# Optimization experiments

Measured on AMD Instinct MI355X. Metric: run time of the kernel, lower is better.

The kernel has to match this reference:

```python
import math
import jax, jax.numpy as jnp
import numpy as np

C = 1.0          # Poincare ball curvature
NUM_HEADS = 8
EPS = 1e-15

def _beta(a, b):
    # Beta function via lgamma (python float constant)
    return math.exp(math.lgamma(a) + math.lgamma(b) - math.lgamma(a + b))

def h_linear(x, z, r, c=C):
    """HNN++ Poincare fully-connected layer (hypll HLinear).
    x: [..., in] points in the ball; z: [in, out] tangent weights; r: [out] bias."""
    sc = math.sqrt(c)
    x2 = jnp.sum(x * x, axis=-1, keepdims=True)
    lam = 2.0 / (1.0 - c * x2)                                # conformal factor
    zn = jnp.maximum(jnp.linalg.norm(z, axis=0), EPS)          # [out]
    inner = x @ z                                              # [..., out]
    two_scr = 2.0 * sc * r
    d = (2.0 * zn / sc) * jnp.arcsinh(
        (sc * inner * lam / zn) * jnp.cosh(two_scr) - (lam - 1.0) * jnp.sinh(two_scr)
    )
    w = jnp.sinh(sc * d) / sc
    return w / (1.0 + jnp.sqrt(1.0 + c * jnp.sum(w * w, axis=-1, keepdims=True)))

def pairwise_dist(q, k, c=C):
    """Poincare distance d(q,k) = arccosh(1 + 2c|q-k|^2 / ((1-c|q|^2)(1-c|k|^2))) / sqrt(c).
    q,k: [B,H,S,hd] -> [B,H,S,S]."""
    q2 = jnp.sum(q * q, axis=-1)
    k2 = jnp.sum(k * k, axis=-1)
    qk = jnp.einsum('bhqd,bhkd->bhqk', q, k)
    diff2 = jnp.maximum(q2[..., :, None] + k2[..., None, :] - 2.0 * qk, 0.0)
    denom = (1.0 - c * q2)[..., :, None] * (1.0 - c * k2)[..., None, :]
    arg = 1.0 + 2.0 * c * diff2 / denom
    return jnp.arccosh(jnp.maximum(arg, 1.0 + 1e-7)) / math.sqrt(c)

def midpoint(v, w, c=C):
    """Weighted Mobius gyromidpoint: m = 1/2 (x) (sum w*lam*x / sum w*(lam-1)).
    v: [B,H,Sk,hd], w: [B,H,Sq,Sk] -> [B,H,Sq,hd]."""
    v2 = jnp.sum(v * v, axis=-1)                      # [B,H,Sk]
    lam = 2.0 / (1.0 - c * v2)
    num = jnp.einsum('bhqk,bhkd->bhqd', w * lam[..., None, :], v)
    den = jnp.maximum(jnp.einsum('bhqk,bhk->bhq', w, lam - 1.0), EPS)[..., None]
    g = num / den                                     # gyromidpoint pre-scaling
    sc = math.sqrt(c)
    gn = jnp.maximum(jnp.linalg.norm(g, axis=-1, keepdims=True), EPS)
    t = jnp.tanh(0.5 * jnp.arctanh(jnp.clip(sc * gn, 0.0, 1.0 - 1e-7)))
    return (t / sc) * g / gn

def _forward(query, key, value, Wq, bq, Wk, bk, Wv, bv, scale_tau, scale_gamma):
    B, S, E = query.shape
    H = NUM_HEADS
    hd = E // H
    # hyperbolic q/k/v projections, then split into heads: [B,H,S,hd]
    q = h_linear(query, Wq, bq).reshape(B, S, H, hd).transpose(0, 2, 1, 3)
    k = h_linear(key, Wk, bk).reshape(B, S, H, hd).transpose(0, 2, 1, 3)
    v = h_linear(value, Wv, bv).reshape(B, S, H, hd).transpose(0, 2, 1, 3)
    # similarity = -dist/tau - gamma with tau = exp(-scale_tau)
    sim = -pairwise_dist(q, k) * jnp.exp(scale_tau[0]) - scale_gamma[0]
    causal = jnp.triu(jnp.ones((S, S), dtype=bool), k=1)
    sim = jnp.where(causal, -jnp.inf, sim)
    w = jnp.exp(sim)                                  # 'exp' attention activation
    agg = midpoint(v, w)                              # [B,H,S,hd]
    agg = agg.transpose(0, 2, 1, 3).reshape(B, S, E)
    # HNN++ beta-concatenation of the per-head ball points
    scale = _beta(E / 2.0, 0.5) / _beta(hd / 2.0, 0.5)
    return agg * scale

def setup_inputs() -> dict:
    root = jax.random.key(0)
    ks = jax.random.split(root, 8)
    B, S, E = 1, 2048, 512
    s = 0.02  # keep points well inside the unit ball
    return {
        'query': s * jax.random.normal(ks[0], (B, S, E), jnp.float32),
        'key':   s * jax.random.normal(ks[1], (B, S, E), jnp.float32),
        'value': s * jax.random.normal(ks[2], (B, S, E), jnp.float32),
        'Wq': s * jax.random.normal(ks[3], (E, E), jnp.float32),
        'Wk': s * jax.random.normal(ks[4], (E, E), jnp.float32),
        'Wv': s * jax.random.normal(ks[5], (E, E), jnp.float32),
        'bq': jnp.zeros((E,), jnp.float32),
        'bk': jnp.zeros((E,), jnp.float32),
        'bv': jnp.zeros((E,), jnp.float32),
        'scale_tau': jnp.zeros((1,), jnp.float32),
        'scale_gamma': jnp.zeros((1,), jnp.float32),
    }

def reference(query, key, value, Wq, Wk, Wv, bq, bk, bv, scale_tau, scale_gamma):
    return _forward(query, key, value, Wq, bq, Wk, bk, Wv, bv, scale_tau, scale_gamma)
```

## Files before the change

kernel.cpp:

```cpp
#include <hip/hip_runtime.h>
#include <cmath>

#define H 8
#define SEQ 2048
#define EDIM 512
#define HD 64
#define EPSF 1e-15f

typedef short bf16x8 __attribute__((ext_vector_type(8)));
typedef float f32x4 __attribute__((ext_vector_type(4)));

#define ZN_OFF    16
#define STATS_OFF (ZN_OFF + 24 * EDIM)
#define CQ_OFF    (STATS_OFF + 3 * H * SEQ)
#define IK_OFF    (CQ_OFF + H * SEQ)
#define PX2_OFF   (IK_OFF + H * SEQ)
#define U16_OFF   (PX2_OFF + 12288 + 16)
#define WT_U16    0
#define QKVB_U16  (WT_U16 + 3 * EDIM * EDIM)
#define VT_U16    (QKVB_U16 + 3 * SEQ * EDIM)
#define U16_TOTAL (VT_U16 + H * 80 * SEQ)
#define BIG_OFF   (U16_OFF + U16_TOTAL / 2 + 16)
#define PART_U16S (8 * 32 * 8 * 4 * 1280)
#define ACC_FLOATS  (H * SEQ * 80)

__device__ __forceinline__ float bf2f(unsigned short u){
  union { unsigned int i; float f; } v; v.i = ((unsigned int)u) << 16; return v.f;
}
__device__ __forceinline__ unsigned short f2bf(float f){
  union { float f; unsigned int i; } v; v.f = f;
  unsigned int x = v.i;
  unsigned int r = (x + 0x7fffu + ((x >> 16) & 1u)) >> 16;
  return (unsigned short)r;
}

__device__ __forceinline__ int detect_f32(const unsigned short* __restrict__ q){
  const int l = threadIdx.x & 63;
  float mx = 0.f;
  #pragma unroll
  for (int j = 0; j < 4; ++j) mx = fmaxf(mx, fabsf(bf2f(q[l * 4 + j])));
  #pragma unroll
  for (int m = 32; m >= 1; m >>= 1) mx = fmaxf(mx, __shfl_xor(mx, m, 64));
  return mx > 1000.f;
}

__global__ __launch_bounds__(256) void wcvt_kernel(
    const void* __restrict__ Wq, const void* __restrict__ Wk, const void* __restrict__ Wv,
    const unsigned short* __restrict__ qprobe,
    unsigned short* __restrict__ WT, float* __restrict__ zn)
{
  const int p = blockIdx.y;
  const int bi = blockIdx.x >> 3, bo = blockIdx.x & 7;
  const void* W = (p == 0) ? Wq : ((p == 1) ? Wk : Wv);
  const int t = threadIdx.x;
  const int isf32 = detect_f32(qprobe);
  __shared__ float tile[64][65];

  #pragma unroll
  for (int j = 0; j < 16; ++j){
    int idx = t + 256 * j;
    int il = idx >> 6, ol = idx & 63;
    float val;
    if (isf32) val = ((const float*)W)[(size_t)(bi * 64 + il) * EDIM + bo * 64 + ol];
    else       val = bf2f(((const unsigned short*)W)[(size_t)(bi * 64 + il) * EDIM + bo * 64 + ol]);
    tile[il][ol] = val;
  }
  __syncthreads();
  if (t < 64){
    float s = 0.f;
    #pragma unroll 8
    for (int i = 0; i < 64; ++i){ float v = tile[i][t]; s += v * v; }
    zn[((size_t)(bi * 3 + p)) * EDIM + bo * 64 + t] = s;
  }
  #pragma unroll
  for (int j = 0; j < 16; ++j){
    int idx = t + 256 * j;
    int ol = idx >> 6, il = idx & 63;
    WT[((size_t)p * EDIM + bo * 64 + ol) * EDIM + bi * 64 + il] = f2bf(tile[il][ol]);
  }
}

__global__ __launch_bounds__(256) void hlin_gemm_kernel(
    const void* __restrict__ Xq, const void* __restrict__ Xk, const void* __restrict__ Xv,
    const unsigned short* __restrict__ WT, const unsigned short* __restrict__ qprobe,
    unsigned short* __restrict__ partC, float* __restrict__ partX2)
{
  const int p = blockIdx.y;
  const int rg = blockIdx.x >> 1;
  const int kslice = blockIdx.x & 1;
  const void* X = (p == 0) ? Xq : ((p == 1) ? Xk : Xv);
  const int r0 = rg * 16;
  const int t  = threadIdx.x;
  const int w = t >> 6, lane = t & 63;
  const int col = lane & 15, quad = lane >> 4;
  const int isf32 = detect_f32(qprobe);
  const int koff = kslice * 256;

  const unsigned short* WTb = WT + ((size_t)p * EDIM + w * 128 + col) * EDIM + koff;
  const float* Xf = (const float*)X + (size_t)(r0 + col) * EDIM + koff;
  const unsigned short* Xh = (const unsigned short*)X + (size_t)(r0 + col) * EDIM + koff;

  f32x4 acc[8];
  #pragma unroll
  for (int nt = 0; nt < 8; ++nt) acc[nt] = (f32x4){0.f, 0.f, 0.f, 0.f};
  float x2part = 0.f;

  bf16x8 caf, naf;
  bf16x8 cbf[8], nbf[8];
  {
    if (isf32){
      float4 xa = *(const float4*)&Xf[quad * 8];
      float4 xb = *(const float4*)&Xf[quad * 8 + 4];
      float xv[8] = {xa.x, xa.y, xa.z, xa.w, xb.x, xb.y, xb.z, xb.w};
      #pragma unroll
      for (int j = 0; j < 8; ++j){ caf[j] = (short)f2bf(xv[j]); x2part += xv[j] * xv[j]; }
    } else {
      caf = *(const bf16x8*)&Xh[quad * 8];
      #pragma unroll
      for (int j = 0; j < 8; ++j){ float xv = bf2f((unsigned short)caf[j]); x2part += xv * xv; }
    }
    #pragma unroll
    for (int nt = 0; nt < 8; ++nt)
      cbf[nt] = *(const bf16x8*)&WTb[(size_t)nt * 16 * EDIM + quad * 8];
  }

  for (int ks = 0; ks < 8; ++ks){
    if (ks + 1 < 8){
      const int off = (ks + 1) * 32 + quad * 8;
      if (isf32){
        float4 xa = *(const float4*)&Xf[off];
        float4 xb = *(const float4*)&Xf[off + 4];
        float xv[8] = {xa.x, xa.y, xa.z, xa.w, xb.x, xb.y, xb.z, xb.w};
        #pragma unroll
        for (int j = 0; j < 8; ++j){ naf[j] = (short)f2bf(xv[j]); x2part += xv[j] * xv[j]; }
      } else {
        naf = *(const bf16x8*)&Xh[off];
        #pragma unroll
        for (int j = 0; j < 8; ++j){ float xv = bf2f((unsigned short)naf[j]); x2part += xv * xv; }
      }
      #pragma unroll
      for (int nt = 0; nt < 8; ++nt)
        nbf[nt] = *(const bf16x8*)&WTb[(size_t)nt * 16 * EDIM + off];
    }
    #pragma unroll
    for (int nt = 0; nt < 8; ++nt)
      acc[nt] = __builtin_amdgcn_mfma_f32_16x16x32_bf16(caf, cbf[nt], acc[nt], 0, 0, 0);
    if (ks + 1 < 8){
      caf = naf;
      #pragma unroll
      for (int nt = 0; nt < 8; ++nt) cbf[nt] = nbf[nt];
    }
  }
  x2part += __shfl_xor(x2part, 16, 64);
  x2part += __shfl_xor(x2part, 32, 64);

  const size_t base = ((size_t)(p * 128 + rg) * 2 + kslice) * 8192;
  #pragma unroll
  for (int nt = 0; nt < 8; ++nt)
    #pragma unroll
    for (int r = 0; r < 4; ++r)
      partC[base + (size_t)(quad * 4 + r) * 512 + w * 128 + nt * 16 + col] = f2bf(acc[nt][r]);
  if (w == 0 && quad == 0)
    partX2[((size_t)(p * 128 + rg) * 2 + kslice) * 16 + col] = x2part;
}

__global__ __launch_bounds__(256) void hlin_fin_kernel(
    const unsigned short* __restrict__ partC, const float* __restrict__ partX2,
    const void* __restrict__ Bq, const void* __restrict__ Bk, const void* __restrict__ Bv,
    const float* __restrict__ znacc, const unsigned short* __restrict__ qprobe,
    unsigned short* __restrict__ qkvb, float* __restrict__ stats,
    float* __restrict__ cqs, float* __restrict__ iks,
    unsigned short* __restrict__ VT)
{
  const int p = blockIdx.y;
  const void* Bb = (p == 0) ? Bq : ((p == 1) ? Bk : Bv);
  const int rg = blockIdx.x;
  const int r0 = rg * 16;
  const int t  = threadIdx.x;
  const int w = t >> 6, lane = t & 63;
  const int col = lane & 15, quad = lane >> 4;
  const int isf32 = detect_f32(qprobe);

  __shared__ float smem[16 * EDIM];
  __shared__ float sw2[16];

  const size_t base0 = ((size_t)(p * 128 + rg) * 2 + 0) * 8192;
  const size_t base1 = base0 + 8192;

  f32x4 acc[8];
  #pragma unroll
  for (int nt = 0; nt < 8; ++nt)
    #pragma unroll
    for (int r = 0; r < 4; ++r){
      const size_t idx = (size_t)(quad * 4 + r) * 512 + w * 128 + nt * 16 + col;
      acc[nt][r] = bf2f(partC[base0 + idx]) + bf2f(partC[base1 + idx]);
    }

  float lamr[4], lm1[4];
  #pragma unroll
  for (int r = 0; r < 4; ++r){
    const int row = quad * 4 + r;
    float x2r = partX2[((size_t)(p * 128 + rg) * 2 + 0) * 16 + row] +
                partX2[((size_t)(p * 128 + rg) * 2 + 1) * 16 + row];
    lamr[r] = 2.f / (1.f - x2r);
    lm1[r] = lamr[r] - 1.f;
  }
  #pragma unroll
  for (int nt = 0; nt < 8; ++nt){
    const int n = w * 128 + nt * 16 + col;
    float zsum = 0.f;
    #pragma unroll
    for (int bi = 0; bi < 8; ++bi)
      zsum += znacc[((size_t)(bi * 3 + p)) * EDIM + n];
    float znv = fmaxf(sqrtf(zsum), EPSF);
    float rb;
    if (isf32) rb = ((const float*)Bb)[n];
    else       rb = bf2f(((const unsigned short*)Bb)[n]);
    float e2r = __expf(2.f * rb);
    float ie2r = 1.f / e2r;
    float ch = 0.5f * (e2r + ie2r), sh = 0.5f * (e2r - ie2r);
    float izn = 1.f / znv;
    float tz = 2.f * znv;
    #pragma unroll
    for (int r = 0; r < 4; ++r){
      float a = (acc[nt][r] * lamr[r] * izn) * ch - lm1[r] * sh;
      float b = a + sqrtf(a * a + 1.f);
      float tt = __expf(tz * __logf(b));
      smem[(quad * 4 + r) * EDIM + n] = 0.5f * (tt - 1.f / tt);
    }
  }
  __syncthreads();

  {
    int row = t >> 4, l = t & 15;
    float s = 0.f;
    for (int o = l; o < EDIM; o += 16){ float wv = smem[row * EDIM + o]; s += wv * wv; }
    #pragma unroll
    for (int m = 8; m >= 1; m >>= 1) s += __shfl_xor(s, m, 16);
    if (l == 0) sw2[row] = s;
  }
  __syncthreads();

  const int o0 = 2 * t;
  const int h0 = t >> 5;
  const int d0 = o0 & 63;
  const int l5 = t & 31;
  #pragma unroll
  for (int rr = 0; rr < 16; ++rr){
    float inv = 1.f / (1.f + sqrtf(1.f + sw2[rr]));
    unsigned short b0 = f2bf(smem[rr * EDIM + o0] * inv);
    unsigned short b1 = f2bf(smem[rr * EDIM + o0 + 1] * inv);
    float r0v = bf2f(b0), r1v = bf2f(b1);
    int s = r0 + rr;
    unsigned int* dst = (unsigned int*)&qkvb[(((size_t)p * H + h0) * SEQ + s) * HD + d0];
    *dst = (unsigned int)b0 | ((unsigned int)b1 << 16);
    float ss = r0v * r0v + r1v * r1v;
    #pragma unroll
    for (int m = 16; m >= 1; m >>= 1) ss += __shfl_xor(ss, m, 64);
    if (p == 2){
      float lam = 2.f / (1.f - ss);
      VT[((size_t)h0 * 80 + d0) * SEQ + s]     = f2bf(r0v * lam);
      VT[((size_t)h0 * 80 + d0 + 1) * SEQ + s] = f2bf(r1v * lam);
      if (l5 < 16)
        VT[((size_t)h0 * 80 + 64 + l5) * SEQ + s] = (l5 == 0) ? f2bf(lam - 1.f) : 0;
    }
    if (l5 == 0){
      stats[((size_t)p * H + h0) * SEQ + s] = ss;
      if (p == 0) cqs[(size_t)h0 * SEQ + s] = 2.f / (1.f - ss);
      if (p == 1) iks[(size_t)h0 * SEQ + s] = 1.f / (1.f - ss);
    }
  }
}

__global__ __launch_bounds__(64) void attn_kernel(
    const unsigned short* __restrict__ Qb, const unsigned short* __restrict__ Kb,
    const unsigned short* __restrict__ VT,
    const float* __restrict__ q2s_all, const float* __restrict__ k2s_all,
    const float* __restrict__ cqs_all, const float* __restrict__ iks_all,
    const void* __restrict__ tau, const void* __restrict__ gam,
    const unsigned short* __restrict__ qprobe,
    float* __restrict__ big, int use_part)
{
  const int h  = blockIdx.y;
  const int tile = 31 - (blockIdx.x >> 4);
  const int sl = (blockIdx.x >> 1) & 7;
  const int wp = blockIdx.x & 1;
  if (sl > tile) return;
  const int lane = threadIdx.x;
  const int col = lane & 15, quad = lane >> 4;
  const int q0A = tile * 64 + wp * 16;
  const int q0B = q0A + 32;

  const unsigned short* Qh  = Qb + (size_t)h * SEQ * HD;
  const unsigned short* Kh  = Kb + (size_t)h * SEQ * HD;
  const unsigned short* VTh = VT + (size_t)h * 80 * SEQ;
  const float* q2s = q2s_all + (size_t)h * SEQ;
  const float* k2s = k2s_all + (size_t)h * SEQ;
  const float* cqs = cqs_all + (size_t)h * SEQ;
  const float* iks = iks_all + (size_t)h * SEQ;

  const int isf32 = detect_f32(qprobe);
  float tauv, gamv;
  if (isf32){ tauv = ((const float*)tau)[0]; gamv = ((const float*)gam)[0]; }
  else      { tauv = bf2f(((const unsigned short*)tau)[0]);
              gamv = bf2f(((const unsigned short*)gam)[0]); }
  const float e_tau = __expf(tauv);

  const int srcA = ((quad & 1) * 2) * 16 + col;
  const int srcB = srcA + 16;
  const int tsel = quad >> 1;

  bf16x8 qfA0 = *(const bf16x8*)&Qh[(size_t)(q0A + col) * HD + quad * 8];
  bf16x8 qfA1 = *(const bf16x8*)&Qh[(size_t)(q0A + col) * HD + 32 + quad * 8];
  bf16x8 qfB0 = *(const bf16x8*)&Qh[(size_t)(q0B + col) * HD + quad * 8];
  bf16x8 qfB1 = *(const bf16x8*)&Qh[(size_t)(q0B + col) * HD + 32 + quad * 8];
  const float q2A = q2s[q0A + col], q2B = q2s[q0B + col];
  const float cqA = cqs[q0A + col], cqB = cqs[q0B + col];
  const int qmaxA = q0A + col, qmaxB = q0B + col;

  f32x4 pvA[5], pvB[5];
  #pragma unroll
  for (int nt = 0; nt < 5; ++nt){
    pvA[nt] = (f32x4){0.f, 0.f, 0.f, 0.f};
    pvB[nt] = (f32x4){0.f, 0.f, 0.f, 0.f};
  }

  const int nch = ((tile - sl) >> 3) + 1;
  const int nhalf = nch * 2;
  int kb32 = sl * 64;

  bf16x8 ckf0[2], ckf1[2], nkf0[2], nkf1[2];
  float4 ck2[2], cik[2], nk2[2], nik[2];
  #pragma unroll
  for (int tt = 0; tt < 2; ++tt){
    const int kbase = kb32 + 16 * tt;
    ckf0[tt] = *(const bf16x8*)&Kh[(size_t)(kbase + col) * HD + quad * 8];
    ckf1[tt] = *(const bf16x8*)&Kh[(size_t)(kbase + col) * HD + 32 + quad * 8];
    ck2[tt]  = *(const float4*)&k2s[kbase + quad * 4];
    cik[tt]  = *(const float4*)&iks[kbase + quad * 4];
  }

  for (int i = 0; i < nhalf; ++i){
    const int nkb32 = (i & 1) ? (kb32 + 512 - 32) : (kb32 + 32);
    const bool have_next = (i + 1 < nhalf);
    if (have_next){
      #pragma unroll
      for (int tt = 0; tt < 2; ++tt){
        const int kbase = nkb32 + 16 * tt;
        nkf0[tt] = *(const bf16x8*)&Kh[(size_t)(kbase + col) * HD + quad * 8];
        nkf1[tt] = *(const bf16x8*)&Kh[(size_t)(kbase + col) * HD + 32 + quad * 8];
        nk2[tt]  = *(const float4*)&k2s[kbase + quad * 4];
        nik[tt]  = *(const float4*)&iks[kbase + quad * 4];
      }
    }

    unsigned int tloA[2], thiA[2], tloB[2], thiB[2];
    #pragma unroll
    for (int tt = 0; tt < 2; ++tt){
      const int kbase = kb32 + 16 * tt;
      f32x4 sA = (f32x4){0.f, 0.f, 0.f, 0.f};
      f32x4 sB = (f32x4){0.f, 0.f, 0.f, 0.f};
      sA = __builtin_amdgcn_mfma_f32_16x16x32_bf16(ckf0[tt], qfA0, sA, 0, 0, 0);
      sB = __builtin_amdgcn_mfma_f32_16x16x32_bf16(ckf0[tt], qfB0, sB, 0, 0, 0);
      sA = __builtin_amdgcn_mfma_f32_16x16x32_bf16(ckf1[tt], qfA1, sA, 0, 0, 0);
      sB = __builtin_amdgcn_mfma_f32_16x16x32_bf16(ckf1[tt], qfB1, sB, 0, 0, 0);
      unsigned short pbA[4], pbB[4];
      #pragma unroll
      for (int r = 0; r < 4; ++r){
        float k2 = (r == 0) ? ck2[tt].x : (r == 1) ? ck2[tt].y : (r == 2) ? ck2[tt].z : ck2[tt].w;
        float ik = (r == 0) ? cik[tt].x : (r == 1) ? cik[tt].y : (r == 2) ? cik[tt].z : cik[tt].w;
        const int key = kbase + quad * 4 + r;
        {
          float diff2 = fmaxf(q2A + k2 - 2.f * sA[r], 0.f);
          float u = fmaxf(diff2 * cqA * ik, 1e-7f);
          float z = 1.f + u + sqrtf(u * (u + 2.f));
          float wv = __expf(-e_tau * __logf(z) - gamv);
          if (key > qmaxA) wv = 0.f;
          pbA[r] = f2bf(wv);
        }
        {
          float diff2 = fmaxf(q2B + k2 - 2.f * sB[r], 0.f);
          float u = fmaxf(diff2 * cqB * ik, 1e-7f);
          float z = 1.f + u + sqrtf(u * (u + 2.f));
          float wv = __expf(-e_tau * __logf(z) - gamv);
          if (key > qmaxB) wv = 0.f;
          pbB[r] = f2bf(wv);
        }
      }
      tloA[tt] = (unsigned int)pbA[0] | ((unsigned int)pbA[1] << 16);
      thiA[tt] = (unsigned int)pbA[2] | ((unsigned int)pbA[3] << 16);
      tloB[tt] = (unsigned int)pbB[0] | ((unsigned int)pbB[1] << 16);
      thiB[tt] = (unsigned int)pbB[2] | ((unsigned int)pbB[3] << 16);
    }
    union { uint4 u; bf16x8 v; } pwA, pwB;
    {
      unsigned int a0 = (unsigned int)__shfl((int)tloA[0], srcA, 64);
      unsigned int a1 = (unsigned int)__shfl((int)tloA[1], srcA, 64);
      unsigned int b0 = (unsigned int)__shfl((int)thiA[0], srcA, 64);
      unsigned int b1 = (unsigned int)__shfl((int)thiA[1], srcA, 64);
      unsigned int c0 = (unsigned int)__shfl((int)tloA[0], srcB, 64);
      unsigned int c1 = (unsigned int)__shfl((int)tloA[1], srcB, 64);
      unsigned int d0 = (unsigned int)__shfl((int)thiA[0], srcB, 64);
      unsigned int d1 = (unsigned int)__shfl((int)thiA[1], srcB, 64);
      pwA.u.x = tsel ? a1 : a0;
      pwA.u.y = tsel ? b1 : b0;
      pwA.u.z = tsel ? c1 : c0;
      pwA.u.w = tsel ? d1 : d0;
    }
    {
      unsigned int a0 = (unsigned int)__shfl((int)tloB[0], srcA, 64);
      unsigned int a1 = (unsigned int)__shfl((int)tloB[1], srcA, 64);
      unsigned int b0 = (unsigned int)__shfl((int)thiB[0], srcA, 64);
      unsigned int b1 = (unsigned int)__shfl((int)thiB[1], srcA, 64);
      unsigned int c0 = (unsigned int)__shfl((int)tloB[0], srcB, 64);
      unsigned int c1 = (unsigned int)__shfl((int)tloB[1], srcB, 64);
      unsigned int d0 = (unsigned int)__shfl((int)thiB[0], srcB, 64);
      unsigned int d1 = (unsigned int)__shfl((int)thiB[1], srcB, 64);
      pwB.u.x = tsel ? a1 : a0;
      pwB.u.y = tsel ? b1 : b0;
      pwB.u.z = tsel ? c1 : c0;
      pwB.u.w = tsel ? d1 : d0;
    }
    #pragma unroll
    for (int nt = 0; nt < 5; ++nt){
      bf16x8 vf = *(const bf16x8*)&VTh[(size_t)(16 * nt + col) * SEQ + kb32 + quad * 8];
      pvA[nt] = __builtin_amdgcn_mfma_f32_16x16x32_bf16(pwA.v, vf, pvA[nt], 0, 0, 0);
      pvB[nt] = __builtin_amdgcn_mfma_f32_16x16x32_bf16(pwB.v, vf, pvB[nt], 0, 0, 0);
    }

    if (have_next){
      #pragma unroll
      for (int tt = 0; tt < 2; ++tt){
        ckf0[tt] = nkf0[tt]; ckf1[tt] = nkf1[tt];
        ck2[tt] = nk2[tt];   cik[tt] = nik[tt];
      }
    }
    kb32 = nkb32;
  }

  if (use_part){
    uint2* slotA = (uint2*)big + (size_t)((((h * 32 + tile) * 8) + sl) * 4 + wp) * 320;
    uint2* slotB = (uint2*)big + (size_t)((((h * 32 + tile) * 8) + sl) * 4 + wp + 2) * 320;
    #pragma unroll
    for (int nt = 0; nt < 5; ++nt){
      uint2 pk;
      pk.x = (unsigned int)f2bf(pvA[nt][0]) | ((unsigned int)f2bf(pvA[nt][1]) << 16);
      pk.y = (unsigned int)f2bf(pvA[nt][2]) | ((unsigned int)f2bf(pvA[nt][3]) << 16);
      slotA[nt * 64 + lane] = pk;
      pk.x = (unsigned int)f2bf(pvB[nt][0]) | ((unsigned int)f2bf(pvB[nt][1]) << 16);
      pk.y = (unsigned int)f2bf(pvB[nt][2]) | ((unsigned int)f2bf(pvB[nt][3]) << 16);
      slotB[nt * 64 + lane] = pk;
    }
  } else {
    #pragma unroll
    for (int r = 0; r < 4; ++r){
      float* rowA = big + ((size_t)h * SEQ + q0A + quad * 4 + r) * 80;
      float* rowB = big + ((size_t)h * SEQ + q0B + quad * 4 + r) * 80;
      #pragma unroll
      for (int nt = 0; nt < 5; ++nt){
        atomicAdd(&rowA[16 * nt + col], pvA[nt][r]);
        atomicAdd(&rowB[16 * nt + col], pvB[nt][r]);
      }
    }
  }
}

__global__ __launch_bounds__(256) void attn_fin_kernel(
    const float* __restrict__ big, int use_part,
    float* __restrict__ out, float beta_scale)
{
  const int h = blockIdx.y, tile16 = blockIdx.x;
  const int t = threadIdx.x;
  const int w = t >> 6, lane = t & 63;
  const int col = lane & 15, quad = lane >> 4;
  const int q0 = tile16 * 16;

  __shared__ float red[4][64][20];

  f32x4 pv[5];
  #pragma unroll
  for (int nt = 0; nt < 5; ++nt) pv[nt] = (f32x4){0.f, 0.f, 0.f, 0.f};

  if (use_part){
    const int st = tile16 >> 2, wq = tile16 & 3;
    const int nv = (st + 1 < 8) ? st + 1 : 8;
    for (int sl = w; sl < nv; sl += 4){
      const uint2* slot = (const uint2*)big +
          (size_t)((((h * 32 + st) * 8) + sl) * 4 + wq) * 320;
      #pragma unroll
      for (int nt = 0; nt < 5; ++nt){
        uint2 v = slot[nt * 64 + lane];
        pv[nt][0] += bf2f((unsigned short)(v.x & 0xffffu));
        pv[nt][1] += bf2f((unsigned short)(v.x >> 16));
        pv[nt][2] += bf2f((unsigned short)(v.y & 0xffffu));
        pv[nt][3] += bf2f((unsigned short)(v.y >> 16));
      }
    }
  } else if (w == 0){
    #pragma unroll
    for (int nt = 0; nt < 5; ++nt)
      #pragma unroll
      for (int r = 0; r < 4; ++r)
        pv[nt][r] = big[((size_t)h * SEQ + q0 + quad * 4 + r) * 80 + 16 * nt + col];
  }

  #pragma unroll
  for (int nt = 0; nt < 5; ++nt)
    *(float4*)&red[w][lane][nt * 4] = (float4){pv[nt][0], pv[nt][1], pv[nt][2], pv[nt][3]};
  __syncthreads();

  if (t < 64){
    #pragma unroll
    for (int nt = 0; nt < 5; ++nt){
      float4 a = *(const float4*)&red[0][t][nt * 4];
      float4 b = *(const float4*)&red[1][t][nt * 4];
      float4 c = *(const float4*)&red[2][t][nt * 4];
      float4 d = *(const float4*)&red[3][t][nt * 4];
      pv[nt][0] = a.x + b.x + c.x + d.x;
      pv[nt][1] = a.y + b.y + c.y + d.y;
      pv[nt][2] = a.z + b.z + c.z + d.z;
      pv[nt][3] = a.w + b.w + c.w + d.w;
    }
    #pragma unroll
    for (int r = 0; r < 4; ++r){
      float den = __shfl(pv[4][r], quad * 16, 64);
      den = fmaxf(den, EPSF);
      float inv_den = 1.f / den;
      float g[4];
      float gsq = 0.f;
      #pragma unroll
      for (int nt = 0; nt < 4; ++nt){ g[nt] = pv[nt][r] * inv_den; gsq += g[nt] * g[nt]; }
      #pragma unroll
      for (int m = 8; m >= 1; m >>= 1) gsq += __shfl_xor(gsq, m, 64);
      float gn = fmaxf(sqrtf(gsq), EPSF);
      float x = fminf(gn, 1.f - 1e-7f);
      float tt2 = x / (1.f + sqrtf(1.f - x * x));
      float scl = (tt2 / gn) * beta_scale;
      const int q = q0 + quad * 4 + r;
      #pragma unroll
      for (int nt = 0; nt < 4; ++nt)
        out[(size_t)q * EDIM + h * HD + 16 * nt + col] = g[nt] * scl;
    }
  }
}

extern "C" void kernel_launch(void* const* d_in, const int* in_sizes, int n_in,
                              void* d_out, int out_size, void* d_ws, size_t ws_size,
                              hipStream_t stream){
  const void* Xq  = d_in[0];
  const void* Xk  = d_in[1];
  const void* Xv  = d_in[2];
  const void* Wq  = d_in[3];
  const void* Wk  = d_in[4];
  const void* Wv  = d_in[5];
  const void* Bq  = d_in[6];
  const void* Bk  = d_in[7];
  const void* Bv  = d_in[8];
  const void* tau = d_in[9];
  const void* gam = d_in[10];

  float* wsf   = (float*)d_ws;
  float* zn    = wsf + ZN_OFF;
  float* stats = wsf + STATS_OFF;
  float* cqs   = wsf + CQ_OFF;
  float* iks   = wsf + IK_OFF;
  float* px2   = wsf + PX2_OFF;
  unsigned short* u16b = (unsigned short*)(wsf + U16_OFF);
  unsigned short* WT   = u16b + WT_U16;
  unsigned short* qkvb = u16b + QKVB_U16;
  unsigned short* VT   = u16b + VT_U16;
  float* big   = wsf + BIG_OFF;
  unsigned short* partC = (unsigned short*)big;

  const int use_part =
      (ws_size >= (size_t)BIG_OFF * sizeof(float) + (size_t)PART_U16S * 2) ? 1 : 0;

  unsigned short* Qb = qkvb;
  unsigned short* Kb = qkvb + (size_t)H * SEQ * HD;
  float* q2s = stats;
  float* k2s = stats + (size_t)H * SEQ;
  const unsigned short* qprobe = (const unsigned short*)Xq;

  double lb1 = lgamma(EDIM / 2.0) + lgamma(0.5) - lgamma(EDIM / 2.0 + 0.5);
  double lb2 = lgamma(HD / 2.0)   + lgamma(0.5) - lgamma(HD / 2.0 + 0.5);
  float beta_scale = (float)exp(lb1 - lb2);

  wcvt_kernel<<<dim3(64, 3), dim3(256), 0, stream>>>(Wq, Wk, Wv, qprobe, WT, zn);
  hlin_gemm_kernel<<<dim3(256, 3), dim3(256), 0, stream>>>(
      Xq, Xk, Xv, WT, qprobe, partC, px2);
  hlin_fin_kernel<<<dim3(128, 3), dim3(256), 0, stream>>>(
      partC, px2, Bq, Bk, Bv, zn, qprobe, qkvb, stats, cqs, iks, VT);
  if (!use_part)
    hipMemsetAsync(big, 0, (size_t)ACC_FLOATS * sizeof(float), stream);
  attn_kernel<<<dim3(32 * 8 * 2, H), dim3(64), 0, stream>>>(
      Qb, Kb, VT, q2s, k2s, cqs, iks, tau, gam, qprobe, big, use_part);
  attn_fin_kernel<<<dim3(128, H), dim3(256), 0, stream>>>(
      big, use_part, (float*)d_out, beta_scale);
}
```

Measured before the change: 202.2 us.

## Split causal attention keys into contiguous 128-wide chunks with triangular partial slots

Before, each attention block handled a strided set of 64-key chunks (stride 512), with 8 split slots per query tile. Now each block processes one contiguous 128-key range, giving up to 16 splits per tile. Partials are stored in a triangular slot layout so the finish kernel reads only the valid slots. The weight computation also uses raw v_log/v_exp/v_sqrt instructions with a folded FMA and packs results with v_cvt_pk_bf16, cutting ALU work. The grid doubles, adding block overhead and more partial traffic in exchange for finer load balance.

Result: faster. 195.0 us (-3.6%).

```diff
diff --git a/kernel.cpp b/kernel.cpp
--- a/kernel.cpp
+++ b/kernel.cpp
@@ -21,7 +21,8 @@
 #define VT_U16    (QKVB_U16 + 3 * SEQ * EDIM)
 #define U16_TOTAL (VT_U16 + H * 80 * SEQ)
 #define BIG_OFF   (U16_OFF + U16_TOTAL / 2 + 16)
-#define PART_U16S (8 * 32 * 8 * 4 * 1280)
+#define TRI_SLOTS 272
+#define PART_U16S (H * TRI_SLOTS * 4 * 1280)
 #define ACC_FLOATS  (H * SEQ * 80)
 
 __device__ __forceinline__ float bf2f(unsigned short u){
@@ -34,6 +35,21 @@
   return (unsigned short)r;
 }
 
+__device__ __forceinline__ unsigned int cvt_pk_bf16(float a, float b){
+  unsigned int r;
+  asm("v_cvt_pk_bf16_f32 %0, %1, %2" : "=v"(r) : "v"(a), "v"(b));
+  return r;
+}
+__device__ __forceinline__ float vlog2f(float x){
+  float r; asm("v_log_f32 %0, %1" : "=v"(r) : "v"(x)); return r;
+}
+__device__ __forceinline__ float vexp2f(float x){
+  float r; asm("v_exp_f32 %0, %1" : "=v"(r) : "v"(x)); return r;
+}
+__device__ __forceinline__ float vsqrtf(float x){
+  float r; asm("v_sqrt_f32 %0, %1" : "=v"(r) : "v"(x)); return r;
+}
+
 __device__ __forceinline__ int detect_f32(const unsigned short* __restrict__ q){
   const int l = threadIdx.x & 63;
   float mx = 0.f;
@@ -42,6 +58,11 @@
   #pragma unroll
   for (int m = 32; m >= 1; m >>= 1) mx = fmaxf(mx, __shfl_xor(mx, m, 64));
   return mx > 1000.f;
+}
+
+__device__ __forceinline__ int tri_base(int t){
+  const int m = t >> 1;
+  return (t & 1) ? (m + 1) * (m + 1) : m * (m + 1);
 }
 
 __global__ __launch_bounds__(256) void wcvt_kernel(
@@ -282,10 +303,15 @@
     float* __restrict__ big, int use_part)
 {
   const int h  = blockIdx.y;
-  const int tile = 31 - (blockIdx.x >> 4);
-  const int sl = (blockIdx.x >> 1) & 7;
+  const int tile = 31 - (blockIdx.x >> 5);
+  const int sl = (blockIdx.x >> 1) & 15;
   const int wp = blockIdx.x & 1;
-  if (sl > tile) return;
+  const int kBeg = sl * 128;
+  const int kEndFull = (tile + 1) * 64;
+  if (kBeg >= kEndFull) return;
+  const int kEnd = (kBeg + 128 < kEndFull) ? (kBeg + 128) : kEndFull;
+  const int nhalf = (kEnd - kBeg) >> 5;
+
   const int lane = threadIdx.x;
   const int col = lane & 15, quad = lane >> 4;
   const int q0A = tile * 64 + wp * 16;
@@ -304,7 +330,8 @@
   if (isf32){ tauv = ((const float*)tau)[0]; gamv = ((const float*)gam)[0]; }
   else      { tauv = bf2f(((const unsigned short*)tau)[0]);
               gamv = bf2f(((const unsigned short*)gam)[0]); }
-  const float e_tau = __expf(tauv);
+  const float m_et = -__expf(tauv);
+  const float m_g2 = -gamv * 1.44269504088896340736f;
 
   const int srcA = ((quad & 1) * 2) * 16 + col;
   const int srcB = srcA + 16;
@@ -325,9 +352,7 @@
     pvB[nt] = (f32x4){0.f, 0.f, 0.f, 0.f};
   }
 
-  const int nch = ((tile - sl) >> 3) + 1;
-  const int nhalf = nch * 2;
-  int kb32 = sl * 64;
+  int kb32 = kBeg;
 
   bf16x8 ckf0[2], ckf1[2], nkf0[2], nkf1[2];
   float4 ck2[2], cik[2], nk2[2], nik[2];
@@ -341,7 +366,7 @@
   }
 
   for (int i = 0; i < nhalf; ++i){
-    const int nkb32 = (i & 1) ? (kb32 + 512 - 32) : (kb32 + 32);
+    const int nkb32 = kb32 + 32;
     const bool have_next = (i + 1 < nhalf);
     if (have_next){
       #pragma unroll
@@ -364,7 +389,7 @@
       sB = __builtin_amdgcn_mfma_f32_16x16x32_bf16(ckf0[tt], qfB0, sB, 0, 0, 0);
       sA = __builtin_amdgcn_mfma_f32_16x16x32_bf16(ckf1[tt], qfA1, sA, 0, 0, 0);
       sB = __builtin_amdgcn_mfma_f32_16x16x32_bf16(ckf1[tt], qfB1, sB, 0, 0, 0);
-      unsigned short pbA[4], pbB[4];
+      float wA[4], wB[4];
       #pragma unroll
       for (int r = 0; r < 4; ++r){
         float k2 = (r == 0) ? ck2[tt].x : (r == 1) ? ck2[tt].y : (r == 2) ? ck2[tt].z : ck2[tt].w;
@@ -373,24 +398,22 @@
         {
           float diff2 = fmaxf(q2A + k2 - 2.f * sA[r], 0.f);
           float u = fmaxf(diff2 * cqA * ik, 1e-7f);
-          float z = 1.f + u + sqrtf(u * (u + 2.f));
-          float wv = __expf(-e_tau * __logf(z) - gamv);
-          if (key > qmaxA) wv = 0.f;
-          pbA[r] = f2bf(wv);
+          float z = 1.f + u + vsqrtf(u * (u + 2.f));
+          float wv = vexp2f(__builtin_fmaf(vlog2f(z), m_et, m_g2));
+          wA[r] = (key > qmaxA) ? 0.f : wv;
         }
         {
           float diff2 = fmaxf(q2B + k2 - 2.f * sB[r], 0.f);
           float u = fmaxf(diff2 * cqB * ik, 1e-7f);
-          float z = 1.f + u + sqrtf(u * (u + 2.f));
-          float wv = __expf(-e_tau * __logf(z) - gamv);
-          if (key > qmaxB) wv = 0.f;
-          pbB[r] = f2bf(wv);
+          float z = 1.f + u + vsqrtf(u * (u + 2.f));
+          float wv = vexp2f(__builtin_fmaf(vlog2f(z), m_et, m_g2));
+          wB[r] = (key > qmaxB) ? 0.f : wv;
         }
       }
-      tloA[tt] = (unsigned int)pbA[0] | ((unsigned int)pbA[1] << 16);
-      thiA[tt] = (unsigned int)pbA[2] | ((unsigned int)pbA[3] << 16);
-      tloB[tt] = (unsigned int)pbB[0] | ((unsigned int)pbB[1] << 16);
-      thiB[tt] = (unsigned int)pbB[2] | ((unsigned int)pbB[3] << 16);
+      tloA[tt] = cvt_pk_bf16(wA[0], wA[1]);
+      thiA[tt] = cvt_pk_bf16(wA[2], wA[3]);
+      tloB[tt] = cvt_pk_bf16(wB[0], wB[1]);
+      thiB[tt] = cvt_pk_bf16(wB[2], wB[3]);
     }
     union { uint4 u; bf16x8 v; } pwA, pwB;
     {
@@ -439,16 +462,17 @@
   }
 
   if (use_part){
-    uint2* slotA = (uint2*)big + (size_t)((((h * 32 + tile) * 8) + sl) * 4 + wp) * 320;
-    uint2* slotB = (uint2*)big + (size_t)((((h * 32 + tile) * 8) + sl) * 4 + wp + 2) * 320;
+    const int tbase = tri_base(tile);
+    uint2* slotA = (uint2*)big + (size_t)(((h * TRI_SLOTS + tbase + sl) * 4) + wp) * 320;
+    uint2* slotB = (uint2*)big + (size_t)(((h * TRI_SLOTS + tbase + sl) * 4) + wp + 2) * 320;
     #pragma unroll
     for (int nt = 0; nt < 5; ++nt){
       uint2 pk;
-      pk.x = (unsigned int)f2bf(pvA[nt][0]) | ((unsigned int)f2bf(pvA[nt][1]) << 16);
-      pk.y = (unsigned int)f2bf(pvA[nt][2]) | ((unsigned int)f2bf(pvA[nt][3]) << 16);
+      pk.x = cvt_pk_bf16(pvA[nt][0], pvA[nt][1]);
+      pk.y = cvt_pk_bf16(pvA[nt][2], pvA[nt][3]);
       slotA[nt * 64 + lane] = pk;
-      pk.x = (unsigned int)f2bf(pvB[nt][0]) | ((unsigned int)f2bf(pvB[nt][1]) << 16);
-      pk.y = (unsigned int)f2bf(pvB[nt][2]) | ((unsigned int)f2bf(pvB[nt][3]) << 16);
+      pk.x = cvt_pk_bf16(pvB[nt][0], pvB[nt][1]);
+      pk.y = cvt_pk_bf16(pvB[nt][2], pvB[nt][3]);
       slotB[nt * 64 + lane] = pk;
     }
   } else {
@@ -483,10 +507,11 @@
 
   if (use_part){
     const int st = tile16 >> 2, wq = tile16 & 3;
-    const int nv = (st + 1 < 8) ? st + 1 : 8;
+    const int tbase = tri_base(st);
+    const int nv = (st + 2) >> 1;
     for (int sl = w; sl < nv; sl += 4){
       const uint2* slot = (const uint2*)big +
-          (size_t)((((h * 32 + st) * 8) + sl) * 4 + wq) * 320;
+          (size_t)((h * TRI_SLOTS + tbase + sl) * 4 + wq) * 320;
       #pragma unroll
       for (int nt = 0; nt < 5; ++nt){
         uint2 v = slot[nt * 64 + lane];
@@ -592,7 +617,7 @@
       partC, px2, Bq, Bk, Bv, zn, qprobe, qkvb, stats, cqs, iks, VT);
   if (!use_part)
     hipMemsetAsync(big, 0, (size_t)ACC_FLOATS * sizeof(float), stream);
-  attn_kernel<<<dim3(32 * 8 * 2, H), dim3(64), 0, stream>>>(
+  attn_kernel<<<dim3(32 * 16 * 2, H), dim3(64), 0, stream>>>(
       Qb, Kb, VT, q2s, k2s, cqs, iks, tau, gam, qprobe, big, use_part);
   attn_fin_kernel<<<dim3(128, H), dim3(256), 0, stream>>>(
       big, use_part, (float*)d_out, beta_scale);
```
